# Kernel optimization log

Measured on AMD Instinct MI355X. Metric: run time of the kernel, lower is better.

Reference implementation:

```python
import math
import jax, jax.numpy as jnp
import numpy as np

B = 32            # batch
C = 64            # prior_feat_channels == fc_hidden_dim
MID = 48          # ROIGather mid_channels
P = 192           # num_priors
S = 36            # sample_points
N_OFFSETS = 72
N_STRIPS = 71
IMG_W, IMG_H = 800, 320
SCALE_FACTOR = 20.0
RH, RW = 10, 25   # FeatureResize target size

SAMPLE_X_IDX = np.floor(np.linspace(0.0, 1.0, S) * N_STRIPS).astype(np.int32)
PRIOR_FEAT_YS = (1.0 - SAMPLE_X_IDX.astype(np.float32) / N_STRIPS)[::-1].copy()
PRIOR_YS = np.linspace(1.0, 0.0, N_OFFSETS, dtype=np.float32)
SX = jnp.asarray(SAMPLE_X_IDX)

def _make_priors():
    pri = np.zeros((P, 6 + N_OFFSETS), np.float32)
    pri[:, 0], pri[:, 1], pri[:, 2] = 0.1, 0.9, 0.5
    pri[:, 3], pri[:, 4], pri[:, 5] = 0.1, 0.0, 50.0
    pri[:, 6:] = ((np.arange(P, dtype=np.float32) + 0.5) / P)[:, None]
    return jnp.asarray(pri)

def _conv1d(x, w, pad):
    # x (N, Cin, L), w (Cout, Cin, K); cross-correlation like torch
    return jax.lax.conv_general_dilated(x, w, (1,), [(pad, pad)], dimension_numbers=('NCH', 'OIH', 'NCH'))

def _resize_nearest(x):
    # F.interpolate(mode='nearest') to (RH, RW), then flatten(2)
    b, c, h, w = x.shape
    hi = (jnp.arange(RH) * h) // RH
    wi = (jnp.arange(RW) * w) // RW
    return x[:, :, hi[:, None], wi[None, :]].reshape(b, c, RH * RW)

def _grid_sample(feat, gx, gy):
    # bilinear, align_corners=True, zeros padding; feat (B,C,H,W), gx/gy (B,P,S)
    b, c, h, w = feat.shape
    ix = (gx + 1.0) * 0.5 * (w - 1)
    iy = (gy + 1.0) * 0.5 * (h - 1)
    x0, y0 = jnp.floor(ix), jnp.floor(iy)
    fflat = feat.reshape(b, c, h * w)
    def corner(xc, yc, wt):
        valid = (xc >= 0) & (xc <= w - 1) & (yc >= 0) & (yc <= h - 1)
        xi = jnp.clip(xc, 0, w - 1).astype(jnp.int32)
        yi = jnp.clip(yc, 0, h - 1).astype(jnp.int32)
        idx = (yi * w + xi).reshape(b, 1, -1)
        v = jnp.take_along_axis(fflat, jnp.broadcast_to(idx, (b, c, idx.shape[-1])), axis=2)
        return v.reshape(b, c, *xc.shape[1:]) * (wt * valid)[:, None]
    return (corner(x0, y0, (x0 + 1 - ix) * (y0 + 1 - iy))
            + corner(x0 + 1, y0, (ix - x0) * (y0 + 1 - iy))
            + corner(x0, y0 + 1, (x0 + 1 - ix) * (iy - y0))
            + corner(x0 + 1, y0 + 1, (ix - x0) * (iy - y0)))


def setup_inputs() -> dict:
    key = jax.random.key(0)
    ks = iter(jax.random.split(key, 64))
    def rn(shape, s=0.05):
        return jax.random.normal(next(ks), shape, jnp.float32) * s
    def ru(shape):
        return jax.random.uniform(next(ks), shape, jnp.float32, 0.5, 1.5)
    return dict(
        feat_s8=rn((B, C, 40, 100), 1.0), feat_s16=rn((B, C, 20, 50), 1.0), feat_s32=rn((B, C, 10, 25), 1.0),
        rg_conv_w=rn((3, MID, C, 9)), rg_conv_scale=ru((3, MID)), rg_conv_bias=rn((3, MID)),
        catconv0_w=rn((C, MID, 9)), catconv1_w=rn((C, 2 * MID, 9)), catconv2_w=rn((C, 3 * MID, 9)),
        catconv_scale=ru((3, C)), catconv_bias=rn((3, C)),
        fc_w=rn((C, C * S)), fc_b=rn((C,)), ln_gamma=ru((C,)), ln_beta=rn((C,)),
        fkey_w=rn((C, C)), fkey_scale=ru((C,)), fkey_bias=rn((C,)),
        fvalue_w=rn((C, C)), fvalue_b=rn((C,)),
        fquery_w=ru((P,)), fquery_b=rn((P,)), attn_w_scale=rn((P,)), attn_w_bias=rn((P,)),
        cls_w1=rn((C, C)), cls_b1=rn((C,)), cls_w2=rn((C, C)), cls_b2=rn((C,)),
        reg_w1=rn((C, C)), reg_b1=rn((C,)), reg_w2=rn((C, C)), reg_b2=rn((C,)),
        cls_head_w=rn((2, C)), cls_head_b=rn((2,)),
        reg_head_w=rn((N_OFFSETS + 4, C)), reg_head_b=rn((N_OFFSETS + 4,)),
        cat_w1=rn((C, C)), cat_b1=rn((C,)), cat_w2=rn((C, C)), cat_b2=rn((C,)),
        prototypes=rn((15, C), 0.01),
        attr_w1=rn((C, C)), attr_b1=rn((C,)), attr_w2=rn((C, C)), attr_b2=rn((C,)),
        attr_head_w=rn((4, C)), attr_head_b=rn((4,)),
    )


def reference(feat_s8, feat_s16, feat_s32, rg_conv_w, rg_conv_scale, rg_conv_bias,
              catconv0_w, catconv1_w, catconv2_w, catconv_scale, catconv_bias,
              fc_w, fc_b, ln_gamma, ln_beta, fkey_w, fkey_scale, fkey_bias,
              fvalue_w, fvalue_b, fquery_w, fquery_b, attn_w_scale, attn_w_bias,
              cls_w1, cls_b1, cls_w2, cls_b2, reg_w1, reg_b1, reg_w2, reg_b2,
              cls_head_w, cls_head_b, reg_head_w, reg_head_b,
              cat_w1, cat_b1, cat_w2, cat_b2, prototypes,
              attr_w1, attr_b1, attr_w2, attr_b2, attr_head_w, attr_head_b):
    relu = jax.nn.relu
    catconv_ws = (catconv0_w, catconv1_w, catconv2_w)
    batch_features = [feat_s32, feat_s16, feat_s8]  # features[-3:] reversed
    priors = jnp.broadcast_to(_make_priors()[None], (B, P, 6 + N_OFFSETS))
    pofm = priors[..., 6 + SX]
    prior_ys = jnp.asarray(PRIOR_YS)
    gy_row = jnp.asarray(PRIOR_FEAT_YS) * 2.0 - 1.0  # (S,)

    roi_stages, predictions, ff_last = [], None, None
    for stage in range(3):
        feat = batch_features[stage]
        prior_xs = jnp.flip(pofm, axis=2)            # (B,P,S)
        gx = prior_xs * 2.0 - 1.0
        gy = jnp.broadcast_to(gy_row[None, None, :], gx.shape)
        pooled = _grid_sample(feat, gx, gy)          # (B,C,P,S)
        pooled = pooled.transpose(0, 2, 1, 3).reshape(B * P, C, S)
        roi_stages.append(pooled)

        # ROIGather.roi_fea: per-stage (9,1) convs (BN folded to scale/bias) + cat conv
        feats = [relu(_conv1d(roi_stages[i], rg_conv_w[i], 4)
                      * rg_conv_scale[i][None, :, None] + rg_conv_bias[i][None, :, None])
                 for i in range(stage + 1)]
        cat_feat = jnp.concatenate(feats, axis=1)
        roi = relu(_conv1d(cat_feat, catconv_ws[stage], 4)
                   * catconv_scale[stage][None, :, None] + catconv_bias[stage][None, :, None])
        # fc + LayerNorm + relu
        roi = roi.reshape(B * P, C * S) @ fc_w.T + fc_b
        mu = roi.mean(-1, keepdims=True)
        var = ((roi - mu) ** 2).mean(-1, keepdims=True)
        roi = (roi - mu) * jax.lax.rsqrt(var + 1e-5) * ln_gamma + ln_beta
        roi = relu(roi).reshape(B, P, C)

        # cross-attention with (nearest-)resized feature map
        key_map = relu(jnp.einsum('bchw,oc->bohw', feat, fkey_w)
                       * fkey_scale[None, :, None, None] + fkey_bias[None, :, None, None])
        key_map = _resize_nearest(key_map)                     # (B,C,N)
        val_map = jnp.einsum('bchw,oc->bohw', feat, fvalue_w) + fvalue_b[None, :, None, None]
        val_map = _resize_nearest(val_map).transpose(0, 2, 1)  # (B,N,C)
        query = relu(roi * fquery_w[None, :, None] + fquery_b[None, :, None])  # grouped 1x1 conv1d
        sim = jax.nn.softmax(jnp.einsum('bpc,bcn->bpn', query, key_map) * (C ** -0.5), axis=-1)
        context = jnp.einsum('bpn,bnc->bpc', sim, val_map)
        context = context * attn_w_scale[None, :, None] + attn_w_bias[None, :, None]
        roi = roi + context

        # faithful to source: view(P,B,C).permute(1,0,2) memory reinterpretation
        ff = roi.reshape(P, B, C).transpose(1, 0, 2).reshape(B * P, C)
        ff_last = ff

        cls_f = relu(ff @ cls_w1.T + cls_b1)
        cls_f = relu(cls_f @ cls_w2.T + cls_b2)
        reg_f = relu(ff @ reg_w1.T + reg_b1)
        reg_f = relu(reg_f @ reg_w2.T + reg_b2)
        cls_logits = (cls_f @ cls_head_w.T + cls_head_b).reshape(B, P, 2)
        reg = (reg_f @ reg_head_w.T + reg_head_b).reshape(B, P, N_OFFSETS + 4)

        p2 = priors[:, :, 2] + reg[:, :, 0]
        p3 = priors[:, :, 3] + reg[:, :, 1]
        p4 = priors[:, :, 4] + reg[:, :, 2]
        p5 = reg[:, :, 3]
        geom = (p3[:, :, None] * (IMG_W - 1)
                + (1.0 - prior_ys[None, None, :] - p2[:, :, None]) * IMG_H
                / jnp.tan(p4[:, :, None] * math.pi + 1e-5)) / (IMG_W - 1)
        lines = jnp.concatenate([cls_logits, p2[..., None], p3[..., None],
                                 p4[..., None], p5[..., None], geom], axis=-1)
        predictions = lines.at[..., 6:].add(reg[:, :, 4:])
        if stage != 2:
            priors = jax.lax.stop_gradient(lines)
            pofm = priors[..., 6 + SX]

    # prototype-based cosine category head (final stage features)
    cat_f = relu(ff_last @ cat_w1.T + cat_b1)
    cat_f = relu(cat_f @ cat_w2.T + cat_b2)
    cat_n = cat_f / jnp.maximum(jnp.linalg.norm(cat_f, axis=-1, keepdims=True), 1e-12)
    proto_n = prototypes / jnp.maximum(jnp.linalg.norm(prototypes, axis=-1, keepdims=True), 1e-12)
    category = (cat_n @ proto_n.T * SCALE_FACTOR).reshape(B, P, -1)
    # left-right attribute head
    attr_f = relu(ff_last @ attr_w1.T + attr_b1)
    attr_f = relu(attr_f @ attr_w2.T + attr_b2)
    attribute = (attr_f @ attr_head_w.T + attr_head_b).reshape(B, P, -1)
    return predictions, category, attribute
```

## Files before the change

### kernel.cpp

```cpp
#include <hip/hip_runtime.h>
#include <math.h>

#define PPRI 192
#define NB   32
#define NS   36
#define BP   6144
#define NPIX 250
#define FPI  3.14159265358979323846f

typedef _Float16 f16x8 __attribute__((ext_vector_type(8)));
typedef float f32x4  __attribute__((ext_vector_type(4)));

__device__ inline short f2h(float x) {
    _Float16 h = (_Float16)x;
    return *(short*)&h;
}
__device__ inline float h2f(short s) {
    _Float16 h = *(_Float16*)&s;
    return (float)h;
}
__device__ inline void splith(float x, short& h, short& l) {
    h = f2h(x); l = f2h(x - h2f(h));
}

__global__ void k_init(float* __restrict__ pofm, float* __restrict__ p234,
                       float* __restrict__ protoN,
                       short* __restrict__ fcBh, short* __restrict__ fcBl,
                       const float* __restrict__ fc_w, const float* __restrict__ protos,
                       short* __restrict__ rgWh, short* __restrict__ rgWl,
                       const float* __restrict__ rg_w,
                       short* __restrict__ catWh, short* __restrict__ catWl,
                       const float* __restrict__ cw0, const float* __restrict__ cw1,
                       const float* __restrict__ cw2) {
    int i = blockIdx.x * 256 + threadIdx.x;
    if (i < BP * NS) {
        int p = (i / NS) % PPRI;
        pofm[i] = ((float)p + 0.5f) / 192.0f;
    }
    if (i < BP) {
        p234[3*i+0] = 0.5f; p234[3*i+1] = 0.1f; p234[3*i+2] = 0.0f;
    }
    if (i < 64 * 2304) {
        int o = i / 2304, k = i % 2304;
        int s = k >> 6, oc = k & 63;
        short h, l; splith(fc_w[o * 2304 + oc * 36 + s], h, l);
        fcBh[i] = h; fcBl[i] = l;
    }
    if (i < 15) {
        float ss = 0.f;
        for (int c = 0; c < 64; ++c) { float v = protos[i*64+c]; ss += v*v; }
        float nrm = fmaxf(sqrtf(ss), 1e-12f);
        for (int c = 0; c < 64; ++c) protoN[i*64+c] = protos[i*64+c] / nrm;
    }
    if (i < 82944) {
        int st = i / 27648, r = i % 27648;
        int k = r / 3072, r2 = r % 3072;
        int oc = r2 / 64, ic = r2 & 63;
        short h, l; splith(rg_w[((st*48 + oc)*64 + ic)*9 + k], h, l);
        rgWh[i] = h; rgWl[i] = l;
    }
    if (i < 184320) {
        int st, base, icw; const float* w;
        if (i < 36864)      { st = 0; base = 0;     icw = 64;  w = cw0; }
        else if (i < 92160) { st = 1; base = 36864; icw = 96;  w = cw1; }
        else                { st = 2; base = 92160; icw = 160; w = cw2; }
        int r = i - base;
        int k = r / (64*icw), r2 = r % (64*icw);
        int oc = r2 / icw, icp = r2 % icw;
        int IC = 48 * (st + 1);
        float wv = (icp < IC) ? w[(oc*IC + icp)*9 + k] : 0.f;
        short h, l; splith(wv, h, l);
        catWh[i] = h; catWl[i] = l;
    }
}

__global__ __launch_bounds__(256) void k_transpose(const float* __restrict__ in,
                                                   float* __restrict__ outT, int HW) {
    __shared__ float t[64][65];
    int b = blockIdx.y;
    int hw0 = blockIdx.x * 64;
    int tx = threadIdx.x & 63, ty = threadIdx.x >> 6;
    const float* ib = in + (size_t)b * 64 * HW;
    for (int c = ty; c < 64; c += 4) {
        int hw = hw0 + tx;
        t[c][tx] = (hw < HW) ? ib[(size_t)c * HW + hw] : 0.f;
    }
    __syncthreads();
    float* ob = outT + (size_t)b * HW * 64;
    for (int r = ty; r < 64; r += 4) {
        int hw = hw0 + r;
        if (hw < HW) ob[(size_t)hw * 64 + tx] = t[tx][r];
    }
}

#define RGWP 80
template<bool SPL>
__global__ __launch_bounds__(192) void k_rgfused(
        const float* __restrict__ featT, int H, int W,
        const float* __restrict__ pofm,
        const short* __restrict__ Wh, const short* __restrict__ Wl,
        const float* __restrict__ scale, const float* __restrict__ bias,
        short* __restrict__ outH, short* __restrict__ outL) {
    constexpr int STG = (SPL ? 2 : 1) * 37 * RGWP;
    constexpr int RED = 9 * 256 * 2;
    constexpr int SMS = (STG > RED) ? STG : RED;
    __shared__ short sm[SMS];
    int tid = threadIdx.x;
    int row = blockIdx.x;
    int wv = tid >> 6, lane = tid & 63;
    int b = row / PPRI;
    float myPof = (lane < 36) ? pofm[row * 36 + lane] : 0.f;
    const float* fb = featT + (size_t)b * H * W * 64;
    for (int si = 0; si < 12; ++si) {
        int s = wv * 12 + si;
        float px = __shfl(myPof, 35 - s);
        px = fminf(fmaxf(px, -1e6f), 1e6f);
        float pfy = (s == 0) ? 0.0f : ((float)(2*s+1) / 71.0f);
        float ix = px  * (float)(W - 1);
        float iy = pfy * (float)(H - 1);
        float x0f = floorf(ix), y0f = floorf(iy);
        float fx = ix - x0f, fy = iy - y0f;
        float vx0 = (x0f >= 0.f     && x0f     <= (float)(W-1)) ? 1.f : 0.f;
        float vx1 = (x0f+1.f >= 0.f && x0f+1.f <= (float)(W-1)) ? 1.f : 0.f;
        float vy0 = (y0f >= 0.f     && y0f     <= (float)(H-1)) ? 1.f : 0.f;
        float vy1 = (y0f+1.f >= 0.f && y0f+1.f <= (float)(H-1)) ? 1.f : 0.f;
        int x0 = min(max((int)x0f, 0), W-1);
        int x1 = min(max((int)x0f + 1, 0), W-1);
        int y0 = min(max((int)y0f, 0), H-1);
        int y1 = min(max((int)y0f + 1, 0), H-1);
        float w00 = (1.f-fx)*(1.f-fy)*vx0*vy0, w10 = fx*(1.f-fy)*vx1*vy0;
        float w01 = (1.f-fx)*fy*vx0*vy1,       w11 = fx*fy*vx1*vy1;
        float v = w00 * fb[(size_t)(y0*W+x0)*64 + lane]
                + w10 * fb[(size_t)(y0*W+x1)*64 + lane]
                + w01 * fb[(size_t)(y1*W+x0)*64 + lane]
                + w11 * fb[(size_t)(y1*W+x1)*64 + lane];
        int di = (s*RGWP + lane) ^ (((s >> 2) & 1) << 3);
        if (SPL) {
            short h, l; splith(v, h, l);
            sm[di] = h;
            sm[37*RGWP + di] = l;
        } else {
            sm[di] = f2h(v);
        }
    }
    if (wv == 0) {
        int di = (36*RGWP + lane) ^ 8;
        sm[di] = 0;
        if (SPL) sm[37*RGWP + di] = 0;
    }
    __syncthreads();
    int lr = lane & 15, kg = lane >> 4;
    const short* shb = sm;
    const short* slb = sm + 37*RGWP;
    f32x4 acc[3][3] = {};
    #pragma unroll
    for (int ssh = 0; ssh < 3; ++ssh) {
        int sh = wv*3 + ssh;
        int sr0 = lr + sh - 4;
        int ar0 = ((unsigned)sr0 < 36u) ? sr0 : 36;
        int ar1 = 16 + lr + sh - 4;
        int sr2 = 32 + lr + sh - 4;
        int ar2 = ((unsigned)sr2 < 36u) ? sr2 : 36;
        int rb0 = ar0*RGWP, rs0 = ((ar0 >> 2) & 1) << 3;
        int rb1 = ar1*RGWP, rs1 = ((ar1 >> 2) & 1) << 3;
        int rb2 = ar2*RGWP, rs2 = ((ar2 >> 2) & 1) << 3;
        #pragma unroll
        for (int kc = 0; kc < 2; ++kc) {
            int icb = kc*32 + kg*8;
            int d0 = (rb0 + icb) ^ rs0;
            int d1 = (rb1 + icb) ^ rs1;
            int d2 = (rb2 + icb) ^ rs2;
            f16x8 ah[3] = { *(const f16x8*)(shb + d0), *(const f16x8*)(shb + d1),
                            *(const f16x8*)(shb + d2) };
            f16x8 al[3];
            if (SPL) {
                al[0] = *(const f16x8*)(slb + d0);
                al[1] = *(const f16x8*)(slb + d1);
                al[2] = *(const f16x8*)(slb + d2);
            }
            const short* wbh = Wh + (size_t)(sh*48)*64 + icb;
            const short* wbl = Wl + (size_t)(sh*48)*64 + icb;
            #pragma unroll
            for (int nt = 0; nt < 3; ++nt) {
                f16x8 bh = *(const f16x8*)(wbh + (nt*16 + lr)*64);
                f16x8 bl;
                if (SPL) bl = *(const f16x8*)(wbl + (nt*16 + lr)*64);
                #pragma unroll
                for (int mt = 0; mt < 3; ++mt) {
                    acc[mt][nt] = __builtin_amdgcn_mfma_f32_16x16x32_f16(ah[mt], bh, acc[mt][nt], 0,0,0);
                    if (SPL) {
                        acc[mt][nt] = __builtin_amdgcn_mfma_f32_16x16x32_f16(ah[mt], bl, acc[mt][nt], 0,0,0);
                        acc[mt][nt] = __builtin_amdgcn_mfma_f32_16x16x32_f16(al[mt], bh, acc[mt][nt], 0,0,0);
                    }
                }
            }
        }
    }
    __syncthreads();
    float* red = (float*)sm;
    if (wv == 2) {
        #pragma unroll
        for (int mt = 0; mt < 3; ++mt)
            #pragma unroll
            for (int nt = 0; nt < 3; ++nt)
                *(f32x4*)(red + ((size_t)(mt*3 + nt))*256 + lane*4) = acc[mt][nt];
    }
    __syncthreads();
    if (wv == 1) {
        #pragma unroll
        for (int mt = 0; mt < 3; ++mt)
            #pragma unroll
            for (int nt = 0; nt < 3; ++nt) {
                f32x4* p = (f32x4*)(red + ((size_t)(mt*3 + nt))*256 + lane*4);
                *p = *p + acc[mt][nt];
            }
    }
    __syncthreads();
    if (wv == 0) {
        #pragma unroll
        for (int nt = 0; nt < 3; ++nt) {
            int oc = nt*16 + lr;
            float sc = scale[oc], bi = bias[oc];
            #pragma unroll
            for (int mt = 0; mt < 3; ++mt) {
                f32x4 a = acc[mt][nt] + *(const f32x4*)(red + ((size_t)(mt*3 + nt))*256 + lane*4);
                #pragma unroll
                for (int i = 0; i < 4; ++i) {
                    int s = mt*16 + kg*4 + i;
                    if (s < 36) {
                        float v = fmaxf(a[i]*sc + bi, 0.f);
                        if (SPL) {
                            short h, l; splith(v, h, l);
                            outH[(size_t)row*36*48 + s*48 + oc] = h;
                            outL[(size_t)row*36*48 + s*48 + oc] = l;
                        } else {
                            outH[(size_t)row*36*48 + s*48 + oc] = f2h(v);
                        }
                    }
                }
            }
        }
    }
}

template<int NC, int NT, int BW, int WP, int ICR, bool SPL>
__global__ __launch_bounds__(192) void k_catconv(
        const short* __restrict__ Xh, const short* __restrict__ Xl,
        const short* __restrict__ Wh, const short* __restrict__ Wl,
        const float* __restrict__ scale, const float* __restrict__ bias,
        short* __restrict__ outH, short* __restrict__ outL) {
    constexpr int icw = NC * 32;
    constexpr int CH  = icw / 8;
    constexpr int STG = (SPL ? 2 : 1) * 37 * WP;
    constexpr int RED = 3 * NT * 256 * 2;
    constexpr int SMS = (STG > RED) ? STG : RED;
    __shared__ short sm[SMS];
    int tid = threadIdx.x;
    int row = blockIdx.x;
    for (int idx = tid; idx < 37*CH; idx += 192) {
        int pos = idx / CH, c0 = (idx % CH) << 3;
        f16x8 h = {}, l = {};
        if (pos < 36 && c0 < ICR) {
            int sidx = c0 / BW, cc = c0 % BW;
            size_t src = ((size_t)(sidx*BP + row)*36 + pos)*BW + cc;
            h = *(const f16x8*)(Xh + src);
            if (SPL) l = *(const f16x8*)(Xl + src);
        }
        int di = (pos*WP + c0) ^ (((pos >> 2) & 1) << 3);
        *(f16x8*)(sm + di) = h;
        if (SPL) *(f16x8*)(sm + 37*WP + di) = l;
    }
    __syncthreads();
    int wv = tid >> 6, lane = tid & 63;
    int lr = lane & 15, kg = lane >> 4;
    const short* shb = sm;
    const short* slb = sm + 37*WP;
    f32x4 acc[3][NT] = {};
    #pragma unroll
    for (int ssh = 0; ssh < 3; ++ssh) {
        int sh = wv*3 + ssh;
        int sr0 = lr + sh - 4;
        int ar0 = ((unsigned)sr0 < 36u) ? sr0 : 36;
        int ar1 = 16 + lr + sh - 4;
        int sr2 = 32 + lr + sh - 4;
        int ar2 = ((unsigned)sr2 < 36u) ? sr2 : 36;
        int rb0 = ar0*WP, rs0 = ((ar0 >> 2) & 1) << 3;
        int rb1 = ar1*WP, rs1 = ((ar1 >> 2) & 1) << 3;
        int rb2 = ar2*WP, rs2 = ((ar2 >> 2) & 1) << 3;
        #pragma unroll
        for (int kc = 0; kc < NC; ++kc) {
            int icb = kc*32 + kg*8;
            int d0 = (rb0 + icb) ^ rs0;
            int d1 = (rb1 + icb) ^ rs1;
            int d2 = (rb2 + icb) ^ rs2;
            f16x8 ah[3] = { *(const f16x8*)(shb + d0), *(const f16x8*)(shb + d1),
                            *(const f16x8*)(shb + d2) };
            f16x8 al[3];
            if (SPL) {
                al[0] = *(const f16x8*)(slb + d0);
                al[1] = *(const f16x8*)(slb + d1);
                al[2] = *(const f16x8*)(slb + d2);
            }
            const short* wbh = Wh + (size_t)(sh*NT*16)*icw + icb;
            const short* wbl = Wl + (size_t)(sh*NT*16)*icw + icb;
            #pragma unroll
            for (int nt = 0; nt < NT; ++nt) {
                f16x8 bh = *(const f16x8*)(wbh + (nt*16 + lr)*icw);
                f16x8 bl;
                if (SPL) bl = *(const f16x8*)(wbl + (nt*16 + lr)*icw);
                #pragma unroll
                for (int mt = 0; mt < 3; ++mt) {
                    acc[mt][nt] = __builtin_amdgcn_mfma_f32_16x16x32_f16(ah[mt], bh, acc[mt][nt], 0,0,0);
                    if (SPL) {
                        acc[mt][nt] = __builtin_amdgcn_mfma_f32_16x16x32_f16(ah[mt], bl, acc[mt][nt], 0,0,0);
                        acc[mt][nt] = __builtin_amdgcn_mfma_f32_16x16x32_f16(al[mt], bh, acc[mt][nt], 0,0,0);
                    }
                }
            }
        }
    }
    __syncthreads();
    float* red = (float*)sm;
    if (wv == 2) {
        #pragma unroll
        for (int mt = 0; mt < 3; ++mt)
            #pragma unroll
            for (int nt = 0; nt < NT; ++nt)
                *(f32x4*)(red + ((size_t)(mt*NT + nt))*256 + lane*4) = acc[mt][nt];
    }
    __syncthreads();
    if (wv == 1) {
        #pragma unroll
        for (int mt = 0; mt < 3; ++mt)
            #pragma unroll
            for (int nt = 0; nt < NT; ++nt) {
                f32x4* p = (f32x4*)(red + ((size_t)(mt*NT + nt))*256 + lane*4);
                *p = *p + acc[mt][nt];
            }
    }
    __syncthreads();
    if (wv == 0) {
        constexpr int OC = NT * 16;
        #pragma unroll
        for (int nt = 0; nt < NT; ++nt) {
            int oc = nt*16 + lr;
            float sc = scale[oc], bi = bias[oc];
            #pragma unroll
            for (int mt = 0; mt < 3; ++mt) {
                f32x4 a = acc[mt][nt] + *(const f32x4*)(red + ((size_t)(mt*NT + nt))*256 + lane*4);
                #pragma unroll
                for (int i = 0; i < 4; ++i) {
                    int s = mt*16 + kg*4 + i;
                    if (s < 36) {
                        float v = fmaxf(a[i]*sc + bi, 0.f);
                        short h, l; splith(v, h, l);
                        outH[(size_t)row*36*OC + s*OC + oc] = h;
                        outL[(size_t)row*36*OC + s*OC + oc] = l;
                    }
                }
            }
        }
    }
}

__global__ __launch_bounds__(256) void k_fc_mfma(
        const short* __restrict__ Ah, const short* __restrict__ Al,
        const short* __restrict__ Bh, const short* __restrict__ Bl,
        const float* __restrict__ fcb,
        const float* __restrict__ gamma, const float* __restrict__ beta,
        float* __restrict__ roi) {
    __shared__ float red[3 * 4 * 256];
    __shared__ float lnb[16][65];
    int tid = threadIdx.x;
    int wv = tid >> 6, lane = tid & 63;
    int lr = lane & 15, kg = lane >> 4;
    int row0 = blockIdx.x * 16;
    f32x4 acc[4] = {};
    for (int kk = 0; kk < 18; ++kk) {
        int k = (wv*18 + kk)*32 + kg*8;
        size_t ar = (size_t)(row0 + lr)*2304 + k;
        f16x8 ah = *(const f16x8*)(Ah + ar);
        f16x8 al = *(const f16x8*)(Al + ar);
        #pragma unroll
        for (int nt = 0; nt < 4; ++nt) {
            size_t br = (size_t)(nt*16 + lr)*2304 + k;
            f16x8 bh = *(const f16x8*)(Bh + br);
            f16x8 bl = *(const f16x8*)(Bl + br);
            acc[nt] = __builtin_amdgcn_mfma_f32_16x16x32_f16(ah, bh, acc[nt], 0,0,0);
            acc[nt] = __builtin_amdgcn_mfma_f32_16x16x32_f16(ah, bl, acc[nt], 0,0,0);
            acc[nt] = __builtin_amdgcn_mfma_f32_16x16x32_f16(al, bh, acc[nt], 0,0,0);
        }
    }
    if (wv > 0) {
        #pragma unroll
        for (int nt = 0; nt < 4; ++nt)
            *(f32x4*)(red + ((size_t)((wv-1)*4 + nt))*256 + lane*4) = acc[nt];
    }
    __syncthreads();
    if (wv == 0) {
        #pragma unroll
        for (int nt = 0; nt < 4; ++nt) {
            f32x4 a = acc[nt]
                    + *(const f32x4*)(red + ((size_t)(0*4 + nt))*256 + lane*4)
                    + *(const f32x4*)(red + ((size_t)(1*4 + nt))*256 + lane*4)
                    + *(const f32x4*)(red + ((size_t)(2*4 + nt))*256 + lane*4);
            #pragma unroll
            for (int i = 0; i < 4; ++i)
                lnb[kg*4 + i][nt*16 + lr] = a[i];
        }
    }
    __syncthreads();
    #pragma unroll
    for (int rr = 0; rr < 4; ++rr) {
        int r = wv*4 + rr;
        float y = lnb[r][lane] + fcb[lane];
        float sum = y;
        #pragma unroll
        for (int off = 32; off > 0; off >>= 1) sum += __shfl_xor(sum, off);
        float mu = sum * (1.f/64.f);
        float d = y - mu;
        float vs = d * d;
        #pragma unroll
        for (int off = 32; off > 0; off >>= 1) vs += __shfl_xor(vs, off);
        float var = vs * (1.f/64.f);
        float outv = d * (1.0f / sqrtf(var + 1e-5f)) * gamma[lane] + beta[lane];
        roi[(size_t)(row0 + r)*64 + lane] = fmaxf(outv, 0.f);
    }
}

__global__ __launch_bounds__(64) void k_keyval(const float* __restrict__ featT, int H, int W,
        const float* __restrict__ kw, const float* __restrict__ ks, const float* __restrict__ kb,
        const float* __restrict__ vw, const float* __restrict__ vb,
        float* __restrict__ keymap, float* __restrict__ valmap) {
    int site = blockIdx.x;
    int b = site / NPIX, n = site % NPIX;
    int r = n / 25, q = n % 25;
    int y = r * H / 10, x = q * W / 25;
    __shared__ float xv[64];
    int tid = threadIdx.x;
    xv[tid] = featT[((size_t)(b * H + y) * W + x) * 64 + tid];
    __syncthreads();
// ... 152 lines not shown
extern "C" void kernel_launch(void* const* d_in, const int* in_sizes, int n_in,
                              void* d_out, int out_size, void* d_ws, size_t ws_size,
                              hipStream_t stream) {
    (void)in_sizes; (void)n_in; (void)out_size; (void)ws_size;
    const float* feat_s8   = (const float*)d_in[0];
    const float* feat_s16  = (const float*)d_in[1];
    const float* feat_s32  = (const float*)d_in[2];
    const float* rg_conv_w     = (const float*)d_in[3];
    const float* rg_conv_scale = (const float*)d_in[4];
    const float* rg_conv_bias  = (const float*)d_in[5];
    const float* catconv_w[3]  = {(const float*)d_in[6], (const float*)d_in[7], (const float*)d_in[8]};
    const float* catconv_scale = (const float*)d_in[9];
    const float* catconv_bias  = (const float*)d_in[10];
    const float* fc_w = (const float*)d_in[11];
    const float* fc_b = (const float*)d_in[12];
    const float* ln_gamma = (const float*)d_in[13];
    const float* ln_beta  = (const float*)d_in[14];
    const float* fkey_w = (const float*)d_in[15];
    const float* fkey_scale = (const float*)d_in[16];
    const float* fkey_bias  = (const float*)d_in[17];
    const float* fvalue_w = (const float*)d_in[18];
    const float* fvalue_b = (const float*)d_in[19];
    const float* fquery_w = (const float*)d_in[20];
    const float* fquery_b = (const float*)d_in[21];
    const float* attn_w_scale = (const float*)d_in[22];
    const float* attn_w_bias  = (const float*)d_in[23];
    const float* cls_w1 = (const float*)d_in[24];
    const float* cls_b1 = (const float*)d_in[25];
    const float* cls_w2 = (const float*)d_in[26];
    const float* cls_b2 = (const float*)d_in[27];
    const float* reg_w1 = (const float*)d_in[28];
    const float* reg_b1 = (const float*)d_in[29];
    const float* reg_w2 = (const float*)d_in[30];
    const float* reg_b2 = (const float*)d_in[31];
    const float* cls_head_w = (const float*)d_in[32];
    const float* cls_head_b = (const float*)d_in[33];
    const float* reg_head_w = (const float*)d_in[34];
    const float* reg_head_b = (const float*)d_in[35];
    const float* cat_w1 = (const float*)d_in[36];
    const float* cat_b1 = (const float*)d_in[37];
    const float* cat_w2 = (const float*)d_in[38];
    const float* cat_b2 = (const float*)d_in[39];
    const float* prototypes = (const float*)d_in[40];
    const float* attr_w1 = (const float*)d_in[41];
    const float* attr_b1 = (const float*)d_in[42];
    const float* attr_w2 = (const float*)d_in[43];
    const float* attr_b2 = (const float*)d_in[44];
    const float* attr_head_w = (const float*)d_in[45];
    const float* attr_head_b = (const float*)d_in[46];

    float* ws = (float*)d_ws;
    float* pofm   = ws;
    float* p234   = ws + 221184;
    float* protoN = ws + 239616;
    short* fcBh   = (short*)(ws + 240576);
    short* fcBl   = (short*)(ws + 314304);
    float* roi    = ws + 388032;
    float* keymap = ws + 781248;
    float* valmap = ws + 1293248;
    short* catHh  = (short*)(ws + 1805248);
    short* catHl  = (short*)(ws + 8883136);
    float* featT  = ws + 15961024;
    short* rgCh   = (short*)(ws + 30116800);
    short* rgCl   = (short*)(ws + 46042048);
    short* rgWh   = (short*)(ws + 61967296);
    short* rgWl   = (short*)(ws + 62008768);
    short* catWh  = (short*)(ws + 62050240);
    short* catWl  = (short*)(ws + 62142400);

    float* out = (float*)d_out;

    k_init<<<864, 256, 0, stream>>>(pofm, p234, protoN, fcBh, fcBl, fc_w, prototypes,
                                    rgWh, rgWl, rg_conv_w, catWh, catWl,
                                    catconv_w[0], catconv_w[1], catconv_w[2]);

    const float* feats[3] = {feat_s32, feat_s16, feat_s8};
    const int Hs[3] = {10, 20, 40}, Wstg[3] = {25, 50, 100};
    const int catbase[3] = {0, 36864, 92160};

    for (int st = 0; st < 3; ++st) {
        int HW = Hs[st] * Wstg[st];
        k_transpose<<<dim3((HW + 63)/64, NB), 256, 0, stream>>>(feats[st], featT, HW);
        if (st < 2)
            k_rgfused<true><<<BP, 192, 0, stream>>>(featT, Hs[st], Wstg[st], pofm,
                                                    rgWh + st*27648, rgWl + st*27648,
                                                    rg_conv_scale + st*48, rg_conv_bias + st*48,
                                                    rgCh + (size_t)st*BP*1728, rgCl + (size_t)st*BP*1728);
        else
            k_rgfused<false><<<BP, 192, 0, stream>>>(featT, Hs[st], Wstg[st], pofm,
                                                     rgWh + st*27648, rgWl + st*27648,
                                                     rg_conv_scale + st*48, rg_conv_bias + st*48,
                                                     rgCh + (size_t)st*BP*1728, rgCl + (size_t)st*BP*1728);
        if (st == 0)
            k_catconv<2,4,48,80,48,true><<<BP, 192, 0, stream>>>(
                    rgCh, rgCl, catWh + catbase[0], catWl + catbase[0],
                    catconv_scale, catconv_bias, catHh, catHl);
        else if (st == 1)
            k_catconv<3,4,48,112,96,true><<<BP, 192, 0, stream>>>(
                    rgCh, rgCl, catWh + catbase[1], catWl + catbase[1],
                    catconv_scale + 64, catconv_bias + 64, catHh, catHl);
        else
            k_catconv<5,4,48,176,144,false><<<BP, 192, 0, stream>>>(
                    rgCh, rgCl, catWh + catbase[2], catWl + catbase[2],
                    catconv_scale + 128, catconv_bias + 128, catHh, catHl);
        k_fc_mfma<<<384, 256, 0, stream>>>(catHh, catHl, fcBh, fcBl,
                                           fc_b, ln_gamma, ln_beta, roi);
        k_keyval<<<NB*NPIX, 64, 0, stream>>>(featT, Hs[st], Wstg[st],
                                             fkey_w, fkey_scale, fkey_bias,
                                             fvalue_w, fvalue_b, keymap, valmap);
        k_attn<<<BP, 256, 0, stream>>>(roi, keymap, valmap, fquery_w, fquery_b,
                                       attn_w_scale, attn_w_bias);
        k_head<<<BP, 128, 0, stream>>>(st, p234, pofm, roi,
                                       reg_w1, reg_b1, reg_w2, reg_b2, reg_head_w, reg_head_b,
                                       cls_w1, cls_b1, cls_w2, cls_b2, cls_head_w, cls_head_b,
                                       out);
    }
    k_catattr<<<BP, 64, 0, stream>>>(roi, cat_w1, cat_b1, cat_w2, cat_b2, protoN,
                                     attr_w1, attr_b1, attr_w2, attr_b2,
                                     attr_head_w, attr_head_b, out);
}
```

Measured before the change: 1.189 ms.

## Assign one prior row per wave in rg and cat conv kernels

Restructures the fused ROI-gather conv and cat-conv kernels so each wave processes a whole row (all 9 kernel taps) instead of three waves splitting the taps of one row. This removes the cross-wave shared-memory reduction and all block-level barriers, and launches a third as many blocks, each with three independent per-wave staging buffers. In exchange each wave does three times the serial MFMA work and sampling loop per row, the tap loop is no longer unrolled, and shared memory per block grows, which could lower occupancy.

```diff
diff --git a/kernel.cpp b/kernel.cpp
--- a/kernel.cpp
+++ b/kernel.cpp
@@ -101,18 +101,16 @@
         const short* __restrict__ Wh, const short* __restrict__ Wl,
         const float* __restrict__ scale, const float* __restrict__ bias,
         short* __restrict__ outH, short* __restrict__ outL) {
-    constexpr int STG = (SPL ? 2 : 1) * 37 * RGWP;
-    constexpr int RED = 9 * 256 * 2;
-    constexpr int SMS = (STG > RED) ? STG : RED;
-    __shared__ short sm[SMS];
+    constexpr int SROW = (SPL ? 2 : 1) * 37 * RGWP;
+    __shared__ short smAll[3 * SROW];
     int tid = threadIdx.x;
-    int row = blockIdx.x;
     int wv = tid >> 6, lane = tid & 63;
+    int row = blockIdx.x * 3 + wv;
+    short* sm = smAll + wv * SROW;
     int b = row / PPRI;
     float myPof = (lane < 36) ? pofm[row * 36 + lane] : 0.f;
     const float* fb = featT + (size_t)b * H * W * 64;
-    for (int si = 0; si < 12; ++si) {
-        int s = wv * 12 + si;
+    for (int s = 0; s < 36; ++s) {
         float px = __shfl(myPof, 35 - s);
         px = fminf(fmaxf(px, -1e6f), 1e6f);
         float pfy = (s == 0) ? 0.0f : ((float)(2*s+1) / 71.0f);
@@ -143,19 +141,16 @@
             sm[di] = f2h(v);
         }
     }
-    if (wv == 0) {
+    {
         int di = (36*RGWP + lane) ^ 8;
         sm[di] = 0;
         if (SPL) sm[37*RGWP + di] = 0;
     }
-    __syncthreads();
     int lr = lane & 15, kg = lane >> 4;
     const short* shb = sm;
     const short* slb = sm + 37*RGWP;
     f32x4 acc[3][3] = {};
-    #pragma unroll
-    for (int ssh = 0; ssh < 3; ++ssh) {
-        int sh = wv*3 + ssh;
+    for (int sh = 0; sh < 9; ++sh) {
         int sr0 = lr + sh - 4;
         int ar0 = ((unsigned)sr0 < 36u) ? sr0 : 36;
         int ar1 = 16 + lr + sh - 4;
@@ -196,46 +191,23 @@
             }
         }
     }
-    __syncthreads();
-    float* red = (float*)sm;
-    if (wv == 2) {
-        #pragma unroll
-        for (int mt = 0; mt < 3; ++mt)
+    #pragma unroll
+    for (int nt = 0; nt < 3; ++nt) {
+        int oc = nt*16 + lr;
+        float sc = scale[oc], bi = bias[oc];
+        #pragma unroll
+        for (int mt = 0; mt < 3; ++mt) {
             #pragma unroll
-            for (int nt = 0; nt < 3; ++nt)
-                *(f32x4*)(red + ((size_t)(mt*3 + nt))*256 + lane*4) = acc[mt][nt];
-    }
-    __syncthreads();
-    if (wv == 1) {
-        #pragma unroll
-        for (int mt = 0; mt < 3; ++mt)
-            #pragma unroll
-            for (int nt = 0; nt < 3; ++nt) {
-                f32x4* p = (f32x4*)(red + ((size_t)(mt*3 + nt))*256 + lane*4);
-                *p = *p + acc[mt][nt];
-            }
-    }
-    __syncthreads();
-    if (wv == 0) {
-        #pragma unroll
-        for (int nt = 0; nt < 3; ++nt) {
-            int oc = nt*16 + lr;
-            float sc = scale[oc], bi = bias[oc];
-            #pragma unroll
-            for (int mt = 0; mt < 3; ++mt) {
-                f32x4 a = acc[mt][nt] + *(const f32x4*)(red + ((size_t)(mt*3 + nt))*256 + lane*4);
-                #pragma unroll
-                for (int i = 0; i < 4; ++i) {
-                    int s = mt*16 + kg*4 + i;
-                    if (s < 36) {
-                        float v = fmaxf(a[i]*sc + bi, 0.f);
-                        if (SPL) {
-                            short h, l; splith(v, h, l);
-                            outH[(size_t)row*36*48 + s*48 + oc] = h;
-                            outL[(size_t)row*36*48 + s*48 + oc] = l;
-                        } else {
-                            outH[(size_t)row*36*48 + s*48 + oc] = f2h(v);
-                        }
+            for (int i = 0; i < 4; ++i) {
+                int s = mt*16 + kg*4 + i;
+                if (s < 36) {
+                    float v = fmaxf(acc[mt][nt][i]*sc + bi, 0.f);
+                    if (SPL) {
+                        short h, l; splith(v, h, l);
+                        outH[(size_t)row*36*48 + s*48 + oc] = h;
+                        outL[(size_t)row*36*48 + s*48 + oc] = l;
+                    } else {
+                        outH[(size_t)row*36*48 + s*48 + oc] = f2h(v);
                     }
                 }
             }
@@ -249,15 +221,15 @@
         const short* __restrict__ Wh, const short* __restrict__ Wl,
         const float* __restrict__ scale, const float* __restrict__ bias,
         short* __restrict__ outH, short* __restrict__ outL) {
-    constexpr int icw = NC * 32;
-    constexpr int CH  = icw / 8;
-    constexpr int STG = (SPL ? 2 : 1) * 37 * WP;
-    constexpr int RED = 3 * NT * 256 * 2;
-    constexpr int SMS = (STG > RED) ? STG : RED;
-    __shared__ short sm[SMS];
+    constexpr int icw  = NC * 32;
+    constexpr int CH   = icw / 8;
+    constexpr int SROW = (SPL ? 2 : 1) * 37 * WP;
+    __shared__ short smAll[3 * SROW];
     int tid = threadIdx.x;
-    int row = blockIdx.x;
-    for (int idx = tid; idx < 37*CH; idx += 192) {
+    int wv = tid >> 6, lane = tid & 63;
+    int row = blockIdx.x * 3 + wv;
+    short* sm = smAll + wv * SROW;
+    for (int idx = lane; idx < 37*CH; idx += 64) {
         int pos = idx / CH, c0 = (idx % CH) << 3;
         f16x8 h = {}, l = {};
         if (pos < 36 && c0 < ICR) {
@@ -270,15 +242,11 @@
         *(f16x8*)(sm + di) = h;
         if (SPL) *(f16x8*)(sm + 37*WP + di) = l;
     }
-    __syncthreads();
-    int wv = tid >> 6, lane = tid & 63;
     int lr = lane & 15, kg = lane >> 4;
     const short* shb = sm;
     const short* slb = sm + 37*WP;
     f32x4 acc[3][NT] = {};
-    #pragma unroll
-    for (int ssh = 0; ssh < 3; ++ssh) {
-        int sh = wv*3 + ssh;
+    for (int sh = 0; sh < 9; ++sh) {
         int sr0 = lr + sh - 4;
         int ar0 = ((unsigned)sr0 < 36u) ? sr0 : 36;
         int ar1 = 16 + lr + sh - 4;
@@ -319,44 +287,21 @@
             }
         }
     }
-    __syncthreads();
-    float* red = (float*)sm;
-    if (wv == 2) {
-        #pragma unroll
-        for (int mt = 0; mt < 3; ++mt)
+    constexpr int OC = NT * 16;
+    #pragma unroll
+    for (int nt = 0; nt < NT; ++nt) {
+        int oc = nt*16 + lr;
+        float sc = scale[oc], bi = bias[oc];
+        #pragma unroll
+        for (int mt = 0; mt < 3; ++mt) {
             #pragma unroll
-            for (int nt = 0; nt < NT; ++nt)
-                *(f32x4*)(red + ((size_t)(mt*NT + nt))*256 + lane*4) = acc[mt][nt];
-    }
-    __syncthreads();
-    if (wv == 1) {
-        #pragma unroll
-        for (int mt = 0; mt < 3; ++mt)
-            #pragma unroll
-            for (int nt = 0; nt < NT; ++nt) {
-                f32x4* p = (f32x4*)(red + ((size_t)(mt*NT + nt))*256 + lane*4);
-                *p = *p + acc[mt][nt];
-            }
-    }
-    __syncthreads();
-    if (wv == 0) {
-        constexpr int OC = NT * 16;
-        #pragma unroll
-        for (int nt = 0; nt < NT; ++nt) {
-            int oc = nt*16 + lr;
-            float sc = scale[oc], bi = bias[oc];
-            #pragma unroll
-            for (int mt = 0; mt < 3; ++mt) {
-                f32x4 a = acc[mt][nt] + *(const f32x4*)(red + ((size_t)(mt*NT + nt))*256 + lane*4);
-                #pragma unroll
-                for (int i = 0; i < 4; ++i) {
-                    int s = mt*16 + kg*4 + i;
-                    if (s < 36) {
-                        float v = fmaxf(a[i]*sc + bi, 0.f);
-                        short h, l; splith(v, h, l);
-                        outH[(size_t)row*36*OC + s*OC + oc] = h;
-                        outL[(size_t)row*36*OC + s*OC + oc] = l;
-                    }
+            for (int i = 0; i < 4; ++i) {
+                int s = mt*16 + kg*4 + i;
+                if (s < 36) {
+                    float v = fmaxf(acc[mt][nt][i]*sc + bi, 0.f);
+                    short h, l; splith(v, h, l);
+                    outH[(size_t)row*36*OC + s*OC + oc] = h;
+                    outL[(size_t)row*36*OC + s*OC + oc] = l;
                 }
             }
         }
@@ -675,25 +620,25 @@
         int HW = Hs[st] * Wstg[st];
         k_transpose<<<dim3((HW + 63)/64, NB), 256, 0, stream>>>(feats[st], featT, HW);
         if (st < 2)
-            k_rgfused<true><<<BP, 192, 0, stream>>>(featT, Hs[st], Wstg[st], pofm,
-                                                    rgWh + st*27648, rgWl + st*27648,
-                                                    rg_conv_scale + st*48, rg_conv_bias + st*48,
-                                                    rgCh + (size_t)st*BP*1728, rgCl + (size_t)st*BP*1728);
+            k_rgfused<true><<<BP/3, 192, 0, stream>>>(featT, Hs[st], Wstg[st], pofm,
+                                                      rgWh + st*27648, rgWl + st*27648,
+                                                      rg_conv_scale + st*48, rg_conv_bias + st*48,
+                                                      rgCh + (size_t)st*BP*1728, rgCl + (size_t)st*BP*1728);
         else
-            k_rgfused<false><<<BP, 192, 0, stream>>>(featT, Hs[st], Wstg[st], pofm,
-                                                     rgWh + st*27648, rgWl + st*27648,
-                                                     rg_conv_scale + st*48, rg_conv_bias + st*48,
-                                                     rgCh + (size_t)st*BP*1728, rgCl + (size_t)st*BP*1728);
+            k_rgfused<false><<<BP/3, 192, 0, stream>>>(featT, Hs[st], Wstg[st], pofm,
+                                                       rgWh + st*27648, rgWl + st*27648,
+                                                       rg_conv_scale + st*48, rg_conv_bias + st*48,
+                                                       rgCh + (size_t)st*BP*1728, rgCl + (size_t)st*BP*1728);
         if (st == 0)
-            k_catconv<2,4,48,80,48,true><<<BP, 192, 0, stream>>>(
+            k_catconv<2,4,48,80,48,true><<<BP/3, 192, 0, stream>>>(
                     rgCh, rgCl, catWh + catbase[0], catWl + catbase[0],
                     catconv_scale, catconv_bias, catHh, catHl);
         else if (st == 1)
-            k_catconv<3,4,48,112,96,true><<<BP, 192, 0, stream>>>(
+            k_catconv<3,4,48,112,96,true><<<BP/3, 192, 0, stream>>>(
                     rgCh, rgCl, catWh + catbase[1], catWl + catbase[1],
                     catconv_scale + 64, catconv_bias + 64, catHh, catHl);
         else
-            k_catconv<5,4,48,176,144,false><<<BP, 192, 0, stream>>>(
+            k_catconv<5,4,48,176,144,false><<<BP/3, 192, 0, stream>>>(
                     rgCh, rgCl, catWh + catbase[2], catWl + catbase[2],
                     catconv_scale + 128, catconv_bias + 128, catHh, catHl);
         k_fc_mfma<<<384, 256, 0, stream>>>(catHh, catHl, fcBh, fcBl,
```

New measurement: 1.289 ms. 1.08x slower.

## Process two prior rows per block in ROI-gather and cat-conv kernels

Applied to the files above, without the earlier changes.

Each block of k_rgfused and k_catconv now handles two consecutive prior rows instead of one, staging both rows in shared memory. Every weight fragment loaded from global memory then feeds MFMAs for both rows, halving weight traffic per row and halving the number of blocks launched. In exchange the accumulator count per thread doubles (register pressure, possibly lower occupancy), and shared memory for staging and reduction doubles.

```diff
diff --git a/kernel.cpp b/kernel.cpp
--- a/kernel.cpp
+++ b/kernel.cpp
@@ -101,19 +101,23 @@
         const short* __restrict__ Wh, const short* __restrict__ Wl,
         const float* __restrict__ scale, const float* __restrict__ bias,
         short* __restrict__ outH, short* __restrict__ outL) {
-    constexpr int STG = (SPL ? 2 : 1) * 37 * RGWP;
-    constexpr int RED = 9 * 256 * 2;
+    constexpr int STGROW = (SPL ? 2 : 1) * 37 * RGWP;
+    constexpr int STG = 2 * STGROW;
+    constexpr int RED = 2 * 9 * 256 * 2;
     constexpr int SMS = (STG > RED) ? STG : RED;
-    __shared__ short sm[SMS];
+    __shared__ short smAll[SMS];
     int tid = threadIdx.x;
-    int row = blockIdx.x;
     int wv = tid >> 6, lane = tid & 63;
-    int b = row / PPRI;
-    float myPof = (lane < 36) ? pofm[row * 36 + lane] : 0.f;
-    const float* fb = featT + (size_t)b * H * W * 64;
-    for (int si = 0; si < 12; ++si) {
-        int s = wv * 12 + si;
-        float px = __shfl(myPof, 35 - s);
+    int row0 = blockIdx.x * 2;
+    float pof0 = (lane < 36) ? pofm[(size_t)row0 * 36 + lane] : 0.f;
+    float pof1 = (lane < 36) ? pofm[(size_t)(row0 + 1) * 36 + lane] : 0.f;
+    for (int j = 0; j < 24; ++j) {
+        int idx = wv * 24 + j;
+        int rl = idx / 36, s = idx % 36;
+        int row = row0 + rl;
+        int b = row / PPRI;
+        const float* fb = featT + (size_t)b * H * W * 64;
+        float px = __shfl(rl ? pof1 : pof0, 35 - s);
         px = fminf(fmaxf(px, -1e6f), 1e6f);
         float pfy = (s == 0) ? 0.0f : ((float)(2*s+1) / 71.0f);
         float ix = px  * (float)(W - 1);
@@ -134,6 +138,7 @@
                 + w10 * fb[(size_t)(y0*W+x1)*64 + lane]
                 + w01 * fb[(size_t)(y1*W+x0)*64 + lane]
                 + w11 * fb[(size_t)(y1*W+x1)*64 + lane];
+        short* sm = smAll + rl * STGROW;
         int di = (s*RGWP + lane) ^ (((s >> 2) & 1) << 3);
         if (SPL) {
             short h, l; splith(v, h, l);
@@ -143,16 +148,16 @@
             sm[di] = f2h(v);
         }
     }
-    if (wv == 0) {
+    if (wv < 2) {
+        short* sm = smAll + wv * STGROW;
         int di = (36*RGWP + lane) ^ 8;
         sm[di] = 0;
         if (SPL) sm[37*RGWP + di] = 0;
     }
     __syncthreads();
     int lr = lane & 15, kg = lane >> 4;
-    const short* shb = sm;
-    const short* slb = sm + 37*RGWP;
-    f32x4 acc[3][3] = {};
+    const short* smr[2] = { smAll, smAll + STGROW };
+    f32x4 acc[2][3][3] = {};
     #pragma unroll
     for (int ssh = 0; ssh < 3; ++ssh) {
         int sh = wv*3 + ssh;
@@ -167,17 +172,15 @@
         #pragma unroll
         for (int kc = 0; kc < 2; ++kc) {
             int icb = kc*32 + kg*8;
-            int d0 = (rb0 + icb) ^ rs0;
-            int d1 = (rb1 + icb) ^ rs1;
-            int d2 = (rb2 + icb) ^ rs2;
-            f16x8 ah[3] = { *(const f16x8*)(shb + d0), *(const f16x8*)(shb + d1),
-                            *(const f16x8*)(shb + d2) };
-            f16x8 al[3];
-            if (SPL) {
-                al[0] = *(const f16x8*)(slb + d0);
-                al[1] = *(const f16x8*)(slb + d1);
-                al[2] = *(const f16x8*)(slb + d2);
-            }
+            int d[3] = { (rb0 + icb) ^ rs0, (rb1 + icb) ^ rs1, (rb2 + icb) ^ rs2 };
+            f16x8 ah[2][3], al[2][3];
+            #pragma unroll
+            for (int r = 0; r < 2; ++r)
+                #pragma unroll
+                for (int mt = 0; mt < 3; ++mt) {
+                    ah[r][mt] = *(const f16x8*)(smr[r] + d[mt]);
+                    if (SPL) al[r][mt] = *(const f16x8*)(smr[r] + 37*RGWP + d[mt]);
+                }
             const short* wbh = Wh + (size_t)(sh*48)*64 + icb;
             const short* wbl = Wl + (size_t)(sh*48)*64 + icb;
             #pragma unroll
@@ -186,55 +189,65 @@
                 f16x8 bl;
                 if (SPL) bl = *(const f16x8*)(wbl + (nt*16 + lr)*64);
                 #pragma unroll
+                for (int r = 0; r < 2; ++r)
+                    #pragma unroll
+                    for (int mt = 0; mt < 3; ++mt) {
+                        acc[r][mt][nt] = __builtin_amdgcn_mfma_f32_16x16x32_f16(ah[r][mt], bh, acc[r][mt][nt], 0,0,0);
+                        if (SPL) {
+                            acc[r][mt][nt] = __builtin_amdgcn_mfma_f32_16x16x32_f16(ah[r][mt], bl, acc[r][mt][nt], 0,0,0);
+                            acc[r][mt][nt] = __builtin_amdgcn_mfma_f32_16x16x32_f16(al[r][mt], bh, acc[r][mt][nt], 0,0,0);
+                        }
+                    }
+            }
+        }
+    }
+    __syncthreads();
+    float* red = (float*)smAll;
+    if (wv == 2) {
+        #pragma unroll
+        for (int r = 0; r < 2; ++r)
+            #pragma unroll
+            for (int mt = 0; mt < 3; ++mt)
+                #pragma unroll
+                for (int nt = 0; nt < 3; ++nt)
+                    *(f32x4*)(red + ((size_t)((r*3 + mt)*3 + nt))*256 + lane*4) = acc[r][mt][nt];
+    }
+    __syncthreads();
+    if (wv == 1) {
+        #pragma unroll
+        for (int r = 0; r < 2; ++r)
+            #pragma unroll
+            for (int mt = 0; mt < 3; ++mt)
+                #pragma unroll
+                for (int nt = 0; nt < 3; ++nt) {
+                    f32x4* p = (f32x4*)(red + ((size_t)((r*3 + mt)*3 + nt))*256 + lane*4);
+                    *p = *p + acc[r][mt][nt];
+                }
+    }
+    __syncthreads();
+    if (wv == 0) {
+        #pragma unroll
+        for (int r = 0; r < 2; ++r) {
+            int row = row0 + r;
+            #pragma unroll
+            for (int nt = 0; nt < 3; ++nt) {
+                int oc = nt*16 + lr;
+                float sc = scale[oc], bi = bias[oc];
+                #pragma unroll
                 for (int mt = 0; mt < 3; ++mt) {
-                    acc[mt][nt] = __builtin_amdgcn_mfma_f32_16x16x32_f16(ah[mt], bh, acc[mt][nt], 0,0,0);
-                    if (SPL) {
-                        acc[mt][nt] = __builtin_amdgcn_mfma_f32_16x16x32_f16(ah[mt], bl, acc[mt][nt], 0,0,0);
-                        acc[mt][nt] = __builtin_amdgcn_mfma_f32_16x16x32_f16(al[mt], bh, acc[mt][nt], 0,0,0);
-                    }
-                }
-            }
-        }
-    }
-    __syncthreads();
-    float* red = (float*)sm;
-    if (wv == 2) {
-        #pragma unroll
-        for (int mt = 0; mt < 3; ++mt)
-            #pragma unroll
-            for (int nt = 0; nt < 3; ++nt)
-                *(f32x4*)(red + ((size_t)(mt*3 + nt))*256 + lane*4) = acc[mt][nt];
-    }
-    __syncthreads();
-    if (wv == 1) {
-        #pragma unroll
-        for (int mt = 0; mt < 3; ++mt)
-            #pragma unroll
-            for (int nt = 0; nt < 3; ++nt) {
-                f32x4* p = (f32x4*)(red + ((size_t)(mt*3 + nt))*256 + lane*4);
-                *p = *p + acc[mt][nt];
-            }
-    }
-    __syncthreads();
-    if (wv == 0) {
-        #pragma unroll
-        for (int nt = 0; nt < 3; ++nt) {
-            int oc = nt*16 + lr;
-            float sc = scale[oc], bi = bias[oc];
-            #pragma unroll
-            for (int mt = 0; mt < 3; ++mt) {
-                f32x4 a = acc[mt][nt] + *(const f32x4*)(red + ((size_t)(mt*3 + nt))*256 + lane*4);
-                #pragma unroll
-                for (int i = 0; i < 4; ++i) {
-                    int s = mt*16 + kg*4 + i;
-                    if (s < 36) {
-                        float v = fmaxf(a[i]*sc + bi, 0.f);
-                        if (SPL) {
-                            short h, l; splith(v, h, l);
-                            outH[(size_t)row*36*48 + s*48 + oc] = h;
-                            outL[(size_t)row*36*48 + s*48 + oc] = l;
-                        } else {
-                            outH[(size_t)row*36*48 + s*48 + oc] = f2h(v);
+                    f32x4 a = acc[r][mt][nt] + *(const f32x4*)(red + ((size_t)((r*3 + mt)*3 + nt))*256 + lane*4);
+                    #pragma unroll
+                    for (int i = 0; i < 4; ++i) {
+                        int s = mt*16 + kg*4 + i;
+                        if (s < 36) {
+                            float v = fmaxf(a[i]*sc + bi, 0.f);
+                            if (SPL) {
+                                short h, l; splith(v, h, l);
+                                outH[(size_t)row*36*48 + s*48 + oc] = h;
+                                outL[(size_t)row*36*48 + s*48 + oc] = l;
+                            } else {
+                                outH[(size_t)row*36*48 + s*48 + oc] = f2h(v);
+                            }
                         }
                     }
                 }
@@ -249,23 +262,26 @@
         const short* __restrict__ Wh, const short* __restrict__ Wl,
         const float* __restrict__ scale, const float* __restrict__ bias,
         short* __restrict__ outH, short* __restrict__ outL) {
-    constexpr int icw = NC * 32;
-    constexpr int CH  = icw / 8;
-    constexpr int STG = (SPL ? 2 : 1) * 37 * WP;
-    constexpr int RED = 3 * NT * 256 * 2;
-    constexpr int SMS = (STG > RED) ? STG : RED;
-    __shared__ short sm[SMS];
+    constexpr int icw  = NC * 32;
+    constexpr int CH   = icw / 8;
+    constexpr int STGROW = (SPL ? 2 : 1) * 37 * WP;
+    constexpr int STG  = 2 * STGROW;
+    constexpr int RED  = 2 * 3 * NT * 256 * 2;
+    constexpr int SMS  = (STG > RED) ? STG : RED;
+    __shared__ short smAll[SMS];
     int tid = threadIdx.x;
-    int row = blockIdx.x;
-    for (int idx = tid; idx < 37*CH; idx += 192) {
-        int pos = idx / CH, c0 = (idx % CH) << 3;
+    int row0 = blockIdx.x * 2;
+    for (int idx = tid; idx < 2*37*CH; idx += 192) {
+        int rl = idx / (37*CH), rem = idx % (37*CH);
+        int pos = rem / CH, c0 = (rem % CH) << 3;
         f16x8 h = {}, l = {};
         if (pos < 36 && c0 < ICR) {
             int sidx = c0 / BW, cc = c0 % BW;
-            size_t src = ((size_t)(sidx*BP + row)*36 + pos)*BW + cc;
+            size_t src = ((size_t)(sidx*BP + row0 + rl)*36 + pos)*BW + cc;
             h = *(const f16x8*)(Xh + src);
             if (SPL) l = *(const f16x8*)(Xl + src);
         }
+        short* sm = smAll + rl * STGROW;
         int di = (pos*WP + c0) ^ (((pos >> 2) & 1) << 3);
         *(f16x8*)(sm + di) = h;
         if (SPL) *(f16x8*)(sm + 37*WP + di) = l;
@@ -273,9 +289,8 @@
     __syncthreads();
     int wv = tid >> 6, lane = tid & 63;
     int lr = lane & 15, kg = lane >> 4;
-    const short* shb = sm;
-    const short* slb = sm + 37*WP;
-    f32x4 acc[3][NT] = {};
+    const short* smr[2] = { smAll, smAll + STGROW };
+    f32x4 acc[2][3][NT] = {};
     #pragma unroll
     for (int ssh = 0; ssh < 3; ++ssh) {
         int sh = wv*3 + ssh;
@@ -290,17 +305,15 @@
         #pragma unroll
         for (int kc = 0; kc < NC; ++kc) {
             int icb = kc*32 + kg*8;
-            int d0 = (rb0 + icb) ^ rs0;
-            int d1 = (rb1 + icb) ^ rs1;
-            int d2 = (rb2 + icb) ^ rs2;
-            f16x8 ah[3] = { *(const f16x8*)(shb + d0), *(const f16x8*)(shb + d1),
-                            *(const f16x8*)(shb + d2) };
-            f16x8 al[3];
-            if (SPL) {
-                al[0] = *(const f16x8*)(slb + d0);
-                al[1] = *(const f16x8*)(slb + d1);
-                al[2] = *(const f16x8*)(slb + d2);
-            }
+            int d[3] = { (rb0 + icb) ^ rs0, (rb1 + icb) ^ rs1, (rb2 + icb) ^ rs2 };
+            f16x8 ah[2][3], al[2][3];
+            #pragma unroll
+            for (int r = 0; r < 2; ++r)
+                #pragma unroll
+                for (int mt = 0; mt < 3; ++mt) {
+                    ah[r][mt] = *(const f16x8*)(smr[r] + d[mt]);
+                    if (SPL) al[r][mt] = *(const f16x8*)(smr[r] + 37*WP + d[mt]);
+                }
             const short* wbh = Wh + (size_t)(sh*NT*16)*icw + icb;
             const short* wbl = Wl + (size_t)(sh*NT*16)*icw + icb;
             #pragma unroll
@@ -309,53 +322,63 @@
                 f16x8 bl;
                 if (SPL) bl = *(const f16x8*)(wbl + (nt*16 + lr)*icw);
                 #pragma unroll
-                for (int mt = 0; mt < 3; ++mt) {
-                    acc[mt][nt] = __builtin_amdgcn_mfma_f32_16x16x32_f16(ah[mt], bh, acc[mt][nt], 0,0,0);
-                    if (SPL) {
-                        acc[mt][nt] = __builtin_amdgcn_mfma_f32_16x16x32_f16(ah[mt], bl, acc[mt][nt], 0,0,0);
-                        acc[mt][nt] = __builtin_amdgcn_mfma_f32_16x16x32_f16(al[mt], bh, acc[mt][nt], 0,0,0);
+                for (int r = 0; r < 2; ++r)
+                    #pragma unroll
+                    for (int mt = 0; mt < 3; ++mt) {
+                        acc[r][mt][nt] = __builtin_amdgcn_mfma_f32_16x16x32_f16(ah[r][mt], bh, acc[r][mt][nt], 0,0,0);
+                        if (SPL) {
+                            acc[r][mt][nt] = __builtin_amdgcn_mfma_f32_16x16x32_f16(ah[r][mt], bl, acc[r][mt][nt], 0,0,0);
+                            acc[r][mt][nt] = __builtin_amdgcn_mfma_f32_16x16x32_f16(al[r][mt], bh, acc[r][mt][nt], 0,0,0);
+                        }
                     }
+            }
+        }
+    }
+    __syncthreads();
+    float* red = (float*)smAll;
+    if (wv == 2) {
+        #pragma unroll
+        for (int r = 0; r < 2; ++r)
+            #pragma unroll
+            for (int mt = 0; mt < 3; ++mt)
+                #pragma unroll
+                for (int nt = 0; nt < NT; ++nt)
+                    *(f32x4*)(red + ((size_t)((r*3 + mt)*NT + nt))*256 + lane*4) = acc[r][mt][nt];
+    }
+    __syncthreads();
+    if (wv == 1) {
+        #pragma unroll
+        for (int r = 0; r < 2; ++r)
+            #pragma unroll
+            for (int mt = 0; mt < 3; ++mt)
+                #pragma unroll
+                for (int nt = 0; nt < NT; ++nt) {
+                    f32x4* p = (f32x4*)(red + ((size_t)((r*3 + mt)*NT + nt))*256 + lane*4);
+                    *p = *p + acc[r][mt][nt];
                 }
-            }
-        }
-    }
-    __syncthreads();
-    float* red = (float*)sm;
-    if (wv == 2) {
-        #pragma unroll
-        for (int mt = 0; mt < 3; ++mt)
-            #pragma unroll
-            for (int nt = 0; nt < NT; ++nt)
-                *(f32x4*)(red + ((size_t)(mt*NT + nt))*256 + lane*4) = acc[mt][nt];
-    }
-    __syncthreads();
-    if (wv == 1) {
-        #pragma unroll
-        for (int mt = 0; mt < 3; ++mt)
-            #pragma unroll
-            for (int nt = 0; nt < NT; ++nt) {
-                f32x4* p = (f32x4*)(red + ((size_t)(mt*NT + nt))*256 + lane*4);
-                *p = *p + acc[mt][nt];
-            }
     }
     __syncthreads();
     if (wv == 0) {
         constexpr int OC = NT * 16;
         #pragma unroll
-        for (int nt = 0; nt < NT; ++nt) {
-            int oc = nt*16 + lr;
-            float sc = scale[oc], bi = bias[oc];
-            #pragma unroll
-            for (int mt = 0; mt < 3; ++mt) {
-                f32x4 a = acc[mt][nt] + *(const f32x4*)(red + ((size_t)(mt*NT + nt))*256 + lane*4);
-                #pragma unroll
-                for (int i = 0; i < 4; ++i) {
-                    int s = mt*16 + kg*4 + i;
-                    if (s < 36) {
-                        float v = fmaxf(a[i]*sc + bi, 0.f);
-                        short h, l; splith(v, h, l);
-                        outH[(size_t)row*36*OC + s*OC + oc] = h;
-                        outL[(size_t)row*36*OC + s*OC + oc] = l;
+        for (int r = 0; r < 2; ++r) {
+            int row = row0 + r;
+            #pragma unroll
+            for (int nt = 0; nt < NT; ++nt) {
+                int oc = nt*16 + lr;
+                float sc = scale[oc], bi = bias[oc];
+                #pragma unroll
+                for (int mt = 0; mt < 3; ++mt) {
+                    f32x4 a = acc[r][mt][nt] + *(const f32x4*)(red + ((size_t)((r*3 + mt)*NT + nt))*256 + lane*4);
+                    #pragma unroll
+                    for (int i = 0; i < 4; ++i) {
+                        int s = mt*16 + kg*4 + i;
+                        if (s < 36) {
+                            float v = fmaxf(a[i]*sc + bi, 0.f);
+                            short h, l; splith(v, h, l);
+                            outH[(size_t)row*36*OC + s*OC + oc] = h;
+                            outL[(size_t)row*36*OC + s*OC + oc] = l;
+                        }
                     }
                 }
             }
@@ -675,25 +698,25 @@
         int HW = Hs[st] * Wstg[st];
         k_transpose<<<dim3((HW + 63)/64, NB), 256, 0, stream>>>(feats[st], featT, HW);
         if (st < 2)
-            k_rgfused<true><<<BP, 192, 0, stream>>>(featT, Hs[st], Wstg[st], pofm,
-                                                    rgWh + st*27648, rgWl + st*27648,
-                                                    rg_conv_scale + st*48, rg_conv_bias + st*48,
-                                                    rgCh + (size_t)st*BP*1728, rgCl + (size_t)st*BP*1728);
+            k_rgfused<true><<<BP/2, 192, 0, stream>>>(featT, Hs[st], Wstg[st], pofm,
+                                                      rgWh + st*27648, rgWl + st*27648,
+                                                      rg_conv_scale + st*48, rg_conv_bias + st*48,
+                                                      rgCh + (size_t)st*BP*1728, rgCl + (size_t)st*BP*1728);
         else
-            k_rgfused<false><<<BP, 192, 0, stream>>>(featT, Hs[st], Wstg[st], pofm,
-                                                     rgWh + st*27648, rgWl + st*27648,
-                                                     rg_conv_scale + st*48, rg_conv_bias + st*48,
-                                                     rgCh + (size_t)st*BP*1728, rgCl + (size_t)st*BP*1728);
+            k_rgfused<false><<<BP/2, 192, 0, stream>>>(featT, Hs[st], Wstg[st], pofm,
+                                                       rgWh + st*27648, rgWl + st*27648,
+                                                       rg_conv_scale + st*48, rg_conv_bias + st*48,
+                                                       rgCh + (size_t)st*BP*1728, rgCl + (size_t)st*BP*1728);
         if (st == 0)
-            k_catconv<2,4,48,80,48,true><<<BP, 192, 0, stream>>>(
+            k_catconv<2,4,48,80,48,true><<<BP/2, 192, 0, stream>>>(
                     rgCh, rgCl, catWh + catbase[0], catWl + catbase[0],
                     catconv_scale, catconv_bias, catHh, catHl);
         else if (st == 1)
-            k_catconv<3,4,48,112,96,true><<<BP, 192, 0, stream>>>(
+            k_catconv<3,4,48,112,96,true><<<BP/2, 192, 0, stream>>>(
                     rgCh, rgCl, catWh + catbase[1], catWl + catbase[1],
                     catconv_scale + 64, catconv_bias + 64, catHh, catHl);
         else
-            k_catconv<5,4,48,176,144,false><<<BP, 192, 0, stream>>>(
+            k_catconv<5,4,48,176,144,false><<<BP/2, 192, 0, stream>>>(
                     rgCh, rgCl, catWh + catbase[2], catWl + catbase[2],
                     catconv_scale + 128, catconv_bias + 128, catHh, catHl);
         k_fc_mfma<<<384, 256, 0, stream>>>(catHh, catHl, fcBh, fcBl,
```

Result: slower. 1.259 ms (+5.9%).
